# Performance work log

Hardware: AMD Instinct MI355X
Metric: run time of the kernel (lower is better)

Reference implementation:

```python
import jax, jax.numpy as jnp
import numpy as np

DIM = 1536
NHEADS = 12
HEADDIM = DIM // NHEADS  # 128
F, H, W = 5, 26, 30
S = F * H * W  # 3900
MAXPOS = 1024
EPS = 1e-6


def setup_inputs() -> dict:
    key = jax.random.key(0)
    ks = jax.random.split(key, 6)
    x = jax.random.normal(ks[0], (1, S, DIM), jnp.float32)
    seq_lens = jnp.array([S], jnp.int32)
    grid_sizes = jnp.array([[F, H, W]], jnp.int32)
    # complex RoPE table as (cos, sin) pairs: [1024, head_dim//2, 2]
    c = HEADDIM // 2
    inv = 1.0 / (10000.0 ** (np.arange(c, dtype=np.float64) / c))
    theta = np.arange(MAXPOS, dtype=np.float64)[:, None] * inv[None, :]
    freqs = jnp.asarray(np.stack([np.cos(theta), np.sin(theta)], axis=-1), jnp.float32)
    scale = 1.0 / np.sqrt(DIM)
    Wq = jax.random.normal(ks[1], (DIM, DIM), jnp.float32) * scale
    Wk = jax.random.normal(ks[2], (DIM, DIM), jnp.float32) * scale
    Wv = jax.random.normal(ks[3], (DIM, DIM), jnp.float32) * scale
    Wo = jax.random.normal(ks[4], (DIM, DIM), jnp.float32) * scale
    bq = jnp.zeros((DIM,), jnp.float32)
    bk = jnp.zeros((DIM,), jnp.float32)
    bv = jnp.zeros((DIM,), jnp.float32)
    bo = jnp.zeros((DIM,), jnp.float32)
    gq = jnp.ones((DIM,), jnp.float32)
    gk = jnp.ones((DIM,), jnp.float32)
    return dict(x=x, seq_lens=seq_lens, grid_sizes=grid_sizes, freqs=freqs,
                Wq=Wq, bq=bq, Wk=Wk, bk=bk, Wv=Wv, bv=bv, Wo=Wo, bo=bo, gq=gq, gk=gk)


def _rms_norm(z, g):
    zf = z.astype(jnp.float32)
    y = zf * jax.lax.rsqrt(jnp.mean(zf * zf, axis=-1, keepdims=True) + EPS)
    return y.astype(z.dtype) * g


def _build_freqs_i(freqs_c, f, h, w):
    # freqs_c: complex [1024, c]; split c into [c-2*(c//3), c//3, c//3] for (F,H,W)
    c = freqs_c.shape[1]
    c3 = c // 3
    c0 = c - 2 * c3
    ff = jnp.broadcast_to(freqs_c[:f, :c0][:, None, None, :], (f, h, w, c0))
    fh = jnp.broadcast_to(freqs_c[:h, c0:c0 + c3][None, :, None, :], (f, h, w, c3))
    fw = jnp.broadcast_to(freqs_c[:w, c0 + c3:][None, None, :, :], (f, h, w, c3))
    return jnp.concatenate([ff, fh, fw], axis=-1).reshape(f * h * w, 1, c)


def _rope_apply(t, freqs_i):
    # t: [1, S, n, d]; interpret last dim as c complex pairs and rotate
    b, s, n, d = t.shape
    c = d // 2
    t2 = t[0].reshape(s, n, c, 2)
    tc = jax.lax.complex(t2[..., 0], t2[..., 1])  # [S, n, c]
    tc = tc * freqs_i  # broadcast [S, 1, c]
    out = jnp.stack([jnp.real(tc), jnp.imag(tc)], axis=-1).reshape(s, n, d)
    return out[None].astype(jnp.float32)


def reference(x, seq_lens, grid_sizes, freqs, Wq, bq, Wk, bk, Wv, bv, Wo, bo, gq, gk):
    b, s, dim = x.shape
    d = freqs.shape[1] * 2  # head_dim
    n = dim // d
    q = _rms_norm(x @ Wq + bq, gq).reshape(b, s, n, d)
    k = _rms_norm(x @ Wk + bk, gk).reshape(b, s, n, d)
    v = (x @ Wv + bv).reshape(b, s, n, d)
    f, h, w = [int(t) for t in np.asarray(grid_sizes)[0]]
    freqs_c = jax.lax.complex(freqs[..., 0], freqs[..., 1])  # [1024, c]
    freqs_i = _build_freqs_i(freqs_c, f, h, w)  # [S, 1, c]
    q = _rope_apply(q, freqs_i)
    k = _rope_apply(k, freqs_i)
    # scaled dot-product attention with key-length mask
    scale = 1.0 / jnp.sqrt(jnp.asarray(d, jnp.float32))
    scores = jnp.einsum('bqnd,bknd->bnqk', q, k) * scale  # [1, n, S, S]
    key_mask = (jnp.arange(s)[None, None, None, :] < seq_lens[:, None, None, None])
    scores = jnp.where(key_mask, scores, jnp.asarray(-1e30, scores.dtype))
    attn = jax.nn.softmax(scores, axis=-1)
    out = jnp.einsum('bnqk,bknd->bqnd', attn, v)  # [1, S, n, d]
    out = out.reshape(b, s, dim)
    return out @ Wo + bo
```

## Files before the change

kernel.cpp:

```cpp
#include <hip/hip_runtime.h>
#include <stdint.h>

#define DIM 1536
#define SLEN 3900
#define SPAD 3904
#define NH 12
#define HD 128
#define SKP 136
#define SVP 68

typedef __bf16 bf16x8 __attribute__((ext_vector_type(8)));
typedef float f32x4 __attribute__((ext_vector_type(4)));

__device__ __forceinline__ float b2f(uint16_t u) {
  union { uint32_t i; float f; } x; x.i = ((uint32_t)u) << 16; return x.f;
}
__device__ __forceinline__ uint16_t f2b(float f) {
  union { __bf16 h; uint16_t u; } c; c.h = (__bf16)f; return c.u;
}
__device__ __forceinline__ bf16x8 ld8bf(const uint16_t* p) {
  bf16x8 r; __builtin_memcpy(&r, p, 16); return r;
}
__device__ __forceinline__ void st8(uint16_t* p, bf16x8 v) {
  __builtin_memcpy(p, &v, 16);
}
__device__ __forceinline__ void gl_lds16(const void* g, void* l) {
  __builtin_amdgcn_global_load_lds((__attribute__((address_space(1))) void*)(g),
                                   (__attribute__((address_space(3))) void*)(l),
                                   16, 0, 0);
}

__global__ __launch_bounds__(256) void conv_x(
    const float* __restrict__ x, uint16_t* __restrict__ xb) {
  int i = (blockIdx.x * 256 + threadIdx.x) * 8;
  float a[8];
  __builtin_memcpy(a, x + i, 32);
  uint16_t t[8];
#pragma unroll
  for (int q = 0; q < 8; q++) t[q] = f2b(a[q]);
  __builtin_memcpy(xb + i, t, 16);
}

__global__ __launch_bounds__(256) void transposeW4(
    const float* __restrict__ w0, const float* __restrict__ w1,
    const float* __restrict__ w2, const float* __restrict__ w3,
    uint16_t* __restrict__ WT4) {
  __shared__ uint16_t t[32][33];
  const int z = blockIdx.z;
  const float* src = z == 0 ? w0 : z == 1 ? w1 : z == 2 ? w2 : w3;
  uint16_t* dst = WT4 + (size_t)z * DIM * DIM;
  const int bx = blockIdx.x * 32, by = blockIdx.y * 32;
  const int tx = threadIdx.x & 31, ty = threadIdx.x >> 5;
#pragma unroll
  for (int i = 0; i < 32; i += 8)
    t[ty + i][tx] = f2b(src[(size_t)(by + ty + i) * DIM + bx + tx]);
  __syncthreads();
#pragma unroll
  for (int i = 0; i < 32; i += 8)
    dst[(size_t)(bx + ty + i) * DIM + by + tx] = t[tx][ty + i];
}

__global__ __launch_bounds__(256) void gemm(
    const uint16_t* __restrict__ A, const uint16_t* __restrict__ BT4,
    uint16_t* __restrict__ Cb, float* __restrict__ Cf,
    const float* __restrict__ bias, int M, int mode) {
  __shared__ __align__(16) uint16_t sA[128 * 32];
  __shared__ __align__(16) uint16_t sB[128 * 32];
  const int z = blockIdx.z;
  const uint16_t* BT = BT4 + (size_t)z * DIM * DIM;
  const int m0 = blockIdx.x * 128;
  const int n0 = blockIdx.y * 128;
  const int tid = threadIdx.x;
  const int wave = tid >> 6, lane = tid & 63;
  const int mh = (wave >> 1) * 64, nh = (wave & 1) * 64;
  const int lr = lane >> 2, lc = (lane & 3) * 8;
  const int r0 = wave * 32;
  const int fm = mh + (lane & 15);
  const int fn = nh + (lane & 15);
  const int ko = (lane >> 4) * 8;

  f32x4 acc[4][4];
  const f32x4 z4 = {0.f, 0.f, 0.f, 0.f};
#pragma unroll
  for (int i = 0; i < 4; i++)
#pragma unroll
    for (int j = 0; j < 4; j++) acc[i][j] = z4;

  for (int k0 = 0; k0 < DIM; k0 += 32) {
    __syncthreads();
#pragma unroll
    for (int j = 0; j < 2; j++) {
      int ra = m0 + r0 + j * 16 + lr; ra = ra < M ? ra : M - 1;
      gl_lds16(A + (size_t)ra * DIM + k0 + lc, (char*)sA + (r0 + j * 16) * 64);
      int rb = n0 + r0 + j * 16 + lr;
      gl_lds16(BT + (size_t)rb * DIM + k0 + lc, (char*)sB + (r0 + j * 16) * 64);
    }
    __builtin_amdgcn_s_waitcnt(0x0f70);
    __syncthreads();
    bf16x8 fa[4], fb[4];
#pragma unroll
    for (int i = 0; i < 4; i++) {
      fa[i] = ld8bf(sA + (fm + i * 16) * 32 + ko);
      fb[i] = ld8bf(sB + (fn + i * 16) * 32 + ko);
    }
#pragma unroll
    for (int i = 0; i < 4; i++)
#pragma unroll
      for (int j = 0; j < 4; j++)
        acc[i][j] = __builtin_amdgcn_mfma_f32_16x16x32_bf16(fa[i], fb[j], acc[i][j], 0, 0, 0);
  }
#pragma unroll
  for (int j = 0; j < 4; j++) {
    int col = n0 + nh + j * 16 + (lane & 15);
    float bvv = (mode == 0 && bias) ? bias[col] : 0.f;
#pragma unroll
    for (int i = 0; i < 4; i++) {
      int row = m0 + mh + i * 16 + (lane >> 4) * 4;
#pragma unroll
      for (int r = 0; r < 4; r++) {
        if (row + r < M) {
          float val = acc[i][j][r] + bvv;
          if (mode == 0)
            Cf[(size_t)(row + r) * DIM + col] = val;
          else
            Cb[(size_t)z * ((size_t)NH * SLEN * HD) +
               (size_t)(col >> 7) * ((size_t)SLEN * HD) +
               (size_t)(row + r) * HD + (col & 127)] = f2b(val);
        }
      }
    }
  }
}

__global__ __launch_bounds__(256) void norm_rope(
    uint16_t* __restrict__ Qb, uint16_t* __restrict__ Kb,
    const float* __restrict__ bq, const float* __restrict__ bk,
    const float* __restrict__ gq, const float* __restrict__ gk,
    const float* __restrict__ freqs, const int* __restrict__ gsz) {
  const int s = blockIdx.x;
  const int isK = blockIdx.y;
  uint32_t* B = (uint32_t*)(isK ? Kb : Qb);
  const float2* br = (const float2*)(isK ? bk : bq);
  const float2* gr = (const float2*)(isK ? gk : gq);
  const int tid = threadIdx.x;
  float va[3], vb[3];
  float ss = 0.f;
#pragma unroll
  for (int i = 0; i < 3; i++) {
    int p = tid + i * 256;
    int h = p >> 6, j = p & 63;
    size_t a = (size_t)h * (SLEN * 64) + (size_t)s * 64 + j;
    uint32_t u = B[a];
    float2 ub = br[p];
    float x0 = b2f((uint16_t)(u & 0xffff)) + ub.x;
    float x1 = b2f((uint16_t)(u >> 16)) + ub.y;
    va[i] = x0; vb[i] = x1; ss += x0 * x0 + x1 * x1;
  }
#pragma unroll
  for (int o = 32; o > 0; o >>= 1) ss += __shfl_down(ss, o, 64);
  __shared__ float red[4];
  if ((tid & 63) == 0) red[tid >> 6] = ss;
  __syncthreads();
  ss = red[0] + red[1] + red[2] + red[3];
  const float rr = rsqrtf(ss * (1.0f / DIM) + 1e-6f);
  const int H = gsz[1], W = gsz[2];
  const int hw = H * W;
  const int fi = s / hw, rem = s - fi * hw;
  const int hi = rem / W, wi = rem - hi * W;
#pragma unroll
  for (int i = 0; i < 3; i++) {
    int p = tid + i * 256;
    int h = p >> 6, j = p & 63;
    int prow = (j < 22) ? fi : (j < 43) ? hi : wi;
    float2 f2 = ((const float2*)freqs)[prow * 64 + j];
    float2 g2 = gr[p];
    float na = va[i] * rr * g2.x;
    float nb = vb[i] * rr * g2.y;
    float ra = na * f2.x - nb * f2.y;
    float rb = na * f2.y + nb * f2.x;
    size_t a = (size_t)h * (SLEN * 64) + (size_t)s * 64 + j;
    B[a] = (uint32_t)f2b(ra) | ((uint32_t)f2b(rb) << 16);
  }
}

__global__ __launch_bounds__(256) void v_reformat(
    const uint16_t* __restrict__ Vb, const float* __restrict__ bv,
    uint16_t* __restrict__ VT) {
  __shared__ uint16_t t[128][136];
  const int head = blockIdx.x;
  const int s0 = blockIdx.y * 128;
  const int tid = threadIdx.x;
  const int cb = (tid & 15) * 8, rb = tid >> 4;
  const uint16_t* Vh = Vb + (size_t)head * SLEN * HD;
  float bvf[8];
#pragma unroll
  for (int q = 0; q < 8; q++) bvf[q] = bv[head * HD + cb + q];
#pragma unroll
  for (int pass = 0; pass < 8; pass++) {
    int r = rb + pass * 16;
    int s = s0 + r; int sc = s < SLEN ? s : SLEN - 1;
    uint16_t u[8];
    __builtin_memcpy(u, Vh + (size_t)sc * HD + cb, 16);
#pragma unroll
    for (int q = 0; q < 8; q++) t[r][cb + q] = f2b(b2f(u[q]) + bvf[q]);
  }
  __syncthreads();
  const int sb = (tid & 15) * 8, db = tid >> 4;
#pragma unroll
  for (int pass = 0; pass < 8; pass++) {
    int d = db + pass * 16;
    uint16_t out[8] __attribute__((aligned(16)));
#pragma unroll
    for (int i2 = 0; i2 < 8; i2++) {
      int s = s0 + sb + i2;
      out[i2] = (s < SLEN) ? t[sb + i2][d] : (uint16_t)0;
    }
    size_t base = ((size_t)head * HD + d) * SPAD + s0 + sb;
    if (s0 + sb + 8 <= SLEN) {
      __builtin_memcpy(VT + base, out, 16);
    } else {
#pragma unroll
      for (int i2 = 0; i2 < 8; i2++) {
        int s = s0 + sb + i2;
        if (s < SPAD) VT[base + i2] = out[i2];
      }
    }
  }
}

__global__ __launch_bounds__(256) void attn(
    const uint16_t* __restrict__ Q, const uint16_t* __restrict__ K,
    const uint16_t* __restrict__ VT, uint16_t* __restrict__ O,
    const int* __restrict__ seq_lens) {
  __shared__ __align__(16) uint16_t sK[64 * SKP];
  __shared__ __align__(16) uint16_t sV[128 * SVP];
  __shared__ __align__(16) uint16_t sP[64 * SVP];
  const int head = blockIdx.x;
  const int q0 = blockIdx.y * 64;
  const int tid = threadIdx.x;
  const int wave = tid >> 6, lane = tid & 63;
  int sl = seq_lens[0];
  const int seqlen = sl < SLEN ? sl : SLEN;
  const uint16_t* Qh = Q + (size_t)head * SLEN * HD;
  const uint16_t* Kh = K + (size_t)head * SLEN * HD;
  const uint16_t* Vh = VT + (size_t)head * HD * SPAD;

  const int fm = lane & 15;
  const int ko = (lane >> 4) * 8;
  const int kr0 = tid >> 4, kcc = (tid & 15) * 8;
  const int vd0 = tid >> 3, vcc = (tid & 7) * 8;

#pragma unroll
  for (int ps = 0; ps < 4; ps++) {
    int row = kr0 + ps * 16;
    int qg = q0 + row; qg = qg < SLEN ? qg : SLEN - 1;
    st8(sK + row * SKP + kcc, ld8bf(Qh + (size_t)qg * HD + kcc));
  }
  __syncthreads();
  bf16x8 aq[4];
#pragma unroll
  for (int kc = 0; kc < 4; kc++)
    aq[kc] = ld8bf(sK + (wave * 16 + fm) * SKP + kc * 32 + ko);

  f32x4 o[8];
  const f32x4 z4 = {0.f, 0.f, 0.f, 0.f};
#pragma unroll
  for (int j = 0; j < 8; j++) o[j] = z4;
  float l_r[4] = {0.f, 0.f, 0.f, 0.f};

  const float C1 = 0.08838834764831845f * 1.4426950408889634f;
  const float C2 = 12.0f * 1.4426950408889634f;

  bf16x8 kr[4], vr[4];
#pragma unroll
  for (int ps = 0; ps < 4; ps++) {
    kr[ps] = ld8bf(Kh + (size_t)(kr0 + ps * 16) * HD + kcc);
    vr[ps] = ld8bf(Vh + (size_t)(vd0 + ps * 32) * SPAD + vcc);
  }

  for (int kv0 = 0; kv0 < SLEN; kv0 += 64) {
    __syncthreads();
#pragma unroll
    for (int ps = 0; ps < 4; ps++) {
      st8(sK + (kr0 + ps * 16) * SKP + kcc, kr[ps]);
      st8(sV + (vd0 + ps * 32) * SVP + vcc, vr[ps]);
    }
    __syncthreads();
    int nv0 = kv0 + 64;
    if (nv0 < SLEN) {
#pragma unroll
      for (int ps = 0; ps < 4; ps++) {
        int kg = nv0 + kr0 + ps * 16; kg = kg < SLEN ? kg : SLEN - 1;
        kr[ps] = ld8bf(Kh + (size_t)kg * HD + kcc);
        vr[ps] = ld8bf(Vh + (size_t)(vd0 + ps * 32) * SPAD + nv0 + vcc);
      }
    }

    f32x4 sc[4];
#pragma unroll
    for (int kk = 0; kk < 4; kk++) sc[kk] = z4;
    __builtin_amdgcn_s_setprio(1);
#pragma unroll
    for (int kc = 0; kc < 4; kc++) {
#pragma unroll
      for (int kk = 0; kk < 4; kk++) {
        bf16x8 bkf = ld8bf(sK + (kk * 16 + fm) * SKP + kc * 32 + ko);
        sc[kk] = __builtin_amdgcn_mfma_f32_16x16x32_bf16(aq[kc], bkf, sc[kk], 0, 0, 0);
      }
    }
    __builtin_amdgcn_s_setprio(0);
#pragma unroll
    for (int kk = 0; kk < 4; kk++) {
      int col = kv0 + kk * 16 + fm;
      bool valid = col < seqlen;
#pragma unroll
      for (int r = 0; r < 4; r++) {
        float p = valid ? exp2f(sc[kk][r] * C1 - C2) : 0.f;
        l_r[r] += p;
        sP[(wave * 16 + (lane >> 4) * 4 + r) * SVP + kk * 16 + fm] = f2b(p);
      }
    }
    __builtin_amdgcn_s_setprio(1);
#pragma unroll
    for (int kc = 0; kc < 2; kc++) {
      bf16x8 ap = ld8bf(sP + (wave * 16 + fm) * SVP + kc * 32 + ko);
#pragma unroll
      for (int j = 0; j < 8; j++) {
        bf16x8 bvf = ld8bf(sV + (j * 16 + fm) * SVP + kc * 32 + ko);
        o[j] = __builtin_amdgcn_mfma_f32_16x16x32_bf16(ap, bvf, o[j], 0, 0, 0);
      }
    }
    __builtin_amdgcn_s_setprio(0);
  }
#pragma unroll
  for (int r = 0; r < 4; r++) {
#pragma unroll
    for (int off = 1; off < 16; off <<= 1) l_r[r] += __shfl_xor(l_r[r], off, 64);
  }
#pragma unroll
  for (int r = 0; r < 4; r++) {
    int row = q0 + wave * 16 + (lane >> 4) * 4 + r;
    if (row < SLEN) {
      float inv = 1.0f / l_r[r];
#pragma unroll
      for (int j = 0; j < 8; j++) {
        int col = head * HD + j * 16 + fm;
        O[(size_t)row * DIM + col] = f2b(o[j][r] * inv);
      }
    }
  }
}

extern "C" void kernel_launch(void* const* d_in, const int* in_sizes, int n_in,
                              void* d_out, int out_size, void* d_ws, size_t ws_size,
                              hipStream_t stream) {
  const float* x      = (const float*)d_in[0];
  const int* seq_lens = (const int*)d_in[1];
  const int* gsz      = (const int*)d_in[2];
  const float* freqs  = (const float*)d_in[3];
  const float* Wq     = (const float*)d_in[4];
  const float* bq     = (const float*)d_in[5];
  const float* Wk     = (const float*)d_in[6];
  const float* bk     = (const float*)d_in[7];
  const float* Wv     = (const float*)d_in[8];
  const float* bv     = (const float*)d_in[9];
  const float* Wo     = (const float*)d_in[10];
  const float* bo     = (const float*)d_in[11];
  const float* gq     = (const float*)d_in[12];
  const float* gk     = (const float*)d_in[13];

  char* p = (char*)d_ws;
  uint16_t* WT4 = (uint16_t*)p; p += (size_t)4 * DIM * DIM * 2;
  uint16_t* Qb  = (uint16_t*)p; p += (size_t)NH * SLEN * HD * 2;
  uint16_t* Kb  = (uint16_t*)p; p += (size_t)NH * SLEN * HD * 2;
  uint16_t* Vb  = (uint16_t*)p; p += (size_t)NH * SLEN * HD * 2;
  uint16_t* VTb = (uint16_t*)p; p += (size_t)NH * HD * SPAD * 2;
  uint16_t* xb  = VTb;
  uint16_t* AO  = Vb;

  conv_x<<<dim3(2925), 256, 0, stream>>>(x, xb);
  transposeW4<<<dim3(48, 48, 4), 256, 0, stream>>>(Wq, Wk, Wv, Wo, WT4);

  gemm<<<dim3(31, 12, 3), 256, 0, stream>>>(xb, WT4, Qb, nullptr, nullptr, SLEN, 1);

  norm_rope<<<dim3(SLEN, 2), 256, 0, stream>>>(Qb, Kb, bq, bk, gq, gk, freqs, gsz);
  v_reformat<<<dim3(NH, 31), 256, 0, stream>>>(Vb, bv, VTb);
  attn<<<dim3(NH, 61), 256, 0, stream>>>(Qb, Kb, VTb, AO, seq_lens);

  gemm<<<dim3(31, 12, 1), 256, 0, stream>>>(AO, WT4 + (size_t)3 * DIM * DIM,
                                            nullptr, (float*)d_out, bo, SLEN, 0);
}
```

Baseline: 469.5 us.

## Keep softmax probabilities in registers via transposed QK MFMA and bpermute

Swaps the MFMA operands for the score product so each lane holds scores for one query column, then packs probabilities with v_cvt_pk_bf16 and shuffles them into the A-operand layout with ds_bpermute. This removes the shared-memory round trip for P and its buffer. It also adds a fast path with no masking for full key tiles and an occupancy hint of 4 blocks per CU. The cost is extra cross-lane permute instructions and inline asm that only targets this ISA.

After: 477.8 us. No clear change (+1.8%).

```diff
diff --git a/kernel.cpp b/kernel.cpp
--- a/kernel.cpp
+++ b/kernel.cpp
@@ -28,6 +28,11 @@
   __builtin_amdgcn_global_load_lds((__attribute__((address_space(1))) void*)(g),
                                    (__attribute__((address_space(3))) void*)(l),
                                    16, 0, 0);
+}
+__device__ __forceinline__ uint32_t cvt_pk_bf16(float a, float b) {
+  uint32_t r;
+  asm("v_cvt_pk_bf16_f32 %0, %1, %2" : "=v"(r) : "v"(a), "v"(b));
+  return r;
 }
 
 __global__ __launch_bounds__(256) void conv_x(
@@ -228,13 +233,12 @@
   }
 }
 
-__global__ __launch_bounds__(256) void attn(
+__global__ __launch_bounds__(256, 4) void attn(
     const uint16_t* __restrict__ Q, const uint16_t* __restrict__ K,
     const uint16_t* __restrict__ VT, uint16_t* __restrict__ O,
     const int* __restrict__ seq_lens) {
   __shared__ __align__(16) uint16_t sK[64 * SKP];
   __shared__ __align__(16) uint16_t sV[128 * SVP];
-  __shared__ __align__(16) uint16_t sP[64 * SVP];
   const int head = blockIdx.x;
   const int q0 = blockIdx.y * 64;
   const int tid = threadIdx.x;
@@ -249,6 +253,9 @@
   const int ko = (lane >> 4) * 8;
   const int kr0 = tid >> 4, kcc = (tid & 15) * 8;
   const int vd0 = tid >> 3, vcc = (tid & 7) * 8;
+  const int addrA = (fm + ((lane & 16) << 1)) * 4;
+  const int addrB = addrA + 64;
+  const int hi_g = (lane >> 5) & 1;
 
 #pragma unroll
   for (int ps = 0; ps < 4; ps++) {
@@ -266,7 +273,7 @@
   const f32x4 z4 = {0.f, 0.f, 0.f, 0.f};
 #pragma unroll
   for (int j = 0; j < 8; j++) o[j] = z4;
-  float l_r[4] = {0.f, 0.f, 0.f, 0.f};
+  float l_part = 0.f;
 
   const float C1 = 0.08838834764831845f * 1.4426950408889634f;
   const float C2 = 12.0f * 1.4426950408889634f;
@@ -305,25 +312,53 @@
 #pragma unroll
       for (int kk = 0; kk < 4; kk++) {
         bf16x8 bkf = ld8bf(sK + (kk * 16 + fm) * SKP + kc * 32 + ko);
-        sc[kk] = __builtin_amdgcn_mfma_f32_16x16x32_bf16(aq[kc], bkf, sc[kk], 0, 0, 0);
+        sc[kk] = __builtin_amdgcn_mfma_f32_16x16x32_bf16(bkf, aq[kc], sc[kk], 0, 0, 0);
       }
     }
     __builtin_amdgcn_s_setprio(0);
-#pragma unroll
-    for (int kk = 0; kk < 4; kk++) {
-      int col = kv0 + kk * 16 + fm;
-      bool valid = col < seqlen;
-#pragma unroll
-      for (int r = 0; r < 4; r++) {
-        float p = valid ? exp2f(sc[kk][r] * C1 - C2) : 0.f;
-        l_r[r] += p;
-        sP[(wave * 16 + (lane >> 4) * 4 + r) * SVP + kk * 16 + fm] = f2b(p);
-      }
-    }
+
+    uint32_t w[4][2];
+    if (kv0 + 64 <= seqlen) {
+#pragma unroll
+      for (int kk = 0; kk < 4; kk++) {
+        float p[4];
+#pragma unroll
+        for (int r = 0; r < 4; r++) {
+          p[r] = exp2f(sc[kk][r] * C1 - C2);
+          l_part += p[r];
+        }
+        w[kk][0] = cvt_pk_bf16(p[0], p[1]);
+        w[kk][1] = cvt_pk_bf16(p[2], p[3]);
+      }
+    } else {
+      const int g4 = (lane >> 4) * 4;
+#pragma unroll
+      for (int kk = 0; kk < 4; kk++) {
+        float p[4];
+#pragma unroll
+        for (int r = 0; r < 4; r++) {
+          int kg = kv0 + kk * 16 + g4 + r;
+          p[r] = (kg < seqlen) ? exp2f(sc[kk][r] * C1 - C2) : 0.f;
+          l_part += p[r];
+        }
+        w[kk][0] = cvt_pk_bf16(p[0], p[1]);
+        w[kk][1] = cvt_pk_bf16(p[2], p[3]);
+      }
+    }
+
     __builtin_amdgcn_s_setprio(1);
 #pragma unroll
     for (int kc = 0; kc < 2; kc++) {
-      bf16x8 ap = ld8bf(sP + (wave * 16 + fm) * SVP + kc * 32 + ko);
+      uint32_t f[4];
+#pragma unroll
+      for (int t = 0; t < 4; t++) {
+        int ad = (t < 2) ? addrA : addrB;
+        uint32_t lo = (uint32_t)__builtin_amdgcn_ds_bpermute(ad, (int)w[2 * kc][t & 1]);
+        uint32_t hi = (uint32_t)__builtin_amdgcn_ds_bpermute(ad, (int)w[2 * kc + 1][t & 1]);
+        f[t] = hi_g ? hi : lo;
+      }
+      bf16x8 ap;
+      __builtin_memcpy(&ap, f, 16);
 #pragma unroll
       for (int j = 0; j < 8; j++) {
         bf16x8 bvf = ld8bf(sV + (j * 16 + fm) * SVP + kc * 32 + ko);
@@ -332,20 +367,21 @@
     }
     __builtin_amdgcn_s_setprio(0);
   }
-#pragma unroll
-  for (int r = 0; r < 4; r++) {
-#pragma unroll
-    for (int off = 1; off < 16; off <<= 1) l_r[r] += __shfl_xor(l_r[r], off, 64);
-  }
+
+  l_part += __shfl_xor(l_part, 16, 64);
+  l_part += __shfl_xor(l_part, 32, 64);
+  float inv[4];
+#pragma unroll
+  for (int r = 0; r < 4; r++)
+    inv[r] = 1.0f / __shfl(l_part, ((lane >> 4) << 2) + r, 64);
 #pragma unroll
   for (int r = 0; r < 4; r++) {
     int row = q0 + wave * 16 + (lane >> 4) * 4 + r;
     if (row < SLEN) {
-      float inv = 1.0f / l_r[r];
 #pragma unroll
       for (int j = 0; j < 8; j++) {
         int col = head * HD + j * 16 + fm;
-        O[(size_t)row * DIM + col] = f2b(o[j][r] * inv);
+        O[(size_t)row * DIM + col] = f2b(o[j][r] * inv[r]);
       }
     }
   }
```
